# Performance work log

Measured on AMD Instinct MI355X. Metric: run time of the kernel, lower is better.

## Reference

```python
import jax, jax.numpy as jnp
import numpy as np

B, CQ, CK, CV, CO = 16, 256, 256, 256, 256
H, W = 80, 80          # query spatial size (P3-like)
KH, KW = 40, 40        # key/value spatial size (P4-like)
HEADS = 4
R2 = 2 * 2             # region_size ** 2
SCALE = 1.0 / np.float32(np.sqrt(CQ))


def conv1x1(x, w, b):
    # 1x1 conv == per-pixel linear map over channels
    return jnp.einsum('bchw,oc->bohw', x, w) + b[None, :, None, None]


def setup_inputs() -> dict:
    key = jax.random.key(0)
    ks = jax.random.split(key, 10)
    s = 0.05
    return {
        'query': jax.random.normal(ks[0], (B, CQ, H, W), jnp.float32),
        'key':   jax.random.normal(ks[1], (B, CK, KH, KW), jnp.float32),
        'wq': jax.random.normal(ks[2], (CQ, CQ), jnp.float32) * s,
        'bq': jax.random.normal(ks[3], (CQ,), jnp.float32) * s,
        'wk': jax.random.normal(ks[4], (CK, CK), jnp.float32) * s,
        'bk': jax.random.normal(ks[5], (CK,), jnp.float32) * s,
        'wv': jax.random.normal(ks[6], (CV, CV), jnp.float32) * s,
        'bv': jax.random.normal(ks[7], (CV,), jnp.float32) * s,
        'wo': jax.random.normal(ks[8], (CO, CV), jnp.float32) * s,
        'bo': jax.random.normal(ks[9], (CO,), jnp.float32) * s,
    }


def reference(query, key, wq, bq, wk, bk, wv, bv, wo, bo):
    # value defaults to key in the original module
    q = conv1x1(query, wq, bq)               # [B,CQ,H,W]
    k = conv1x1(key, wk, bk)                 # [B,CK,KH,KW]
    v = conv1x1(key, wv, bv)                 # [B,CV,KH,KW]

    b, cq, h, w = q.shape
    # All R2 'patches' in the source are the SAME interpolation (no offsets),
    # so compute it once; bilinear resize matches torch align_corners=False.
    ki = jax.image.resize(k, (b, k.shape[1], h, w), method='bilinear')
    vi = jax.image.resize(v, (b, v.shape[1], h, w), method='bilinear')

    q5 = q.reshape(b, HEADS, cq // HEADS, h, w)
    k5 = ki.reshape(b, HEADS, k.shape[1] // HEADS, h, w)
    v5 = vi.reshape(b, HEADS, v.shape[1] // HEADS, h, w)

    # per-region score; identical for every region patch
    score = jnp.einsum('bhcxy,bhcxy->bhxy', q5, k5) * SCALE     # [B,h,H,W]
    scores = jnp.broadcast_to(score[:, :, None], (b, HEADS, R2, h, w))
    # NOTE: original uses nn.Softmax(dim=3) -> normalizes over the H axis
    attn = jax.nn.softmax(scores, axis=3)                       # [B,h,R2,H,W]

    # out = sum over regions of attn * v (v identical across regions)
    out = jnp.einsum('bhrxy,bhcxy->bhcxy', attn, v5)            # [B,h,C/h,H,W]
    out = out.reshape(b, -1, h, w)                              # [B,CV,H,W]
    return conv1x1(out, wo, bo)                                 # [B,CO,H,W]
```

## Files before the change

kernel.cpp:

```cpp
#include <hip/hip_runtime.h>
#include <hip/hip_bf16.h>

typedef __bf16 bf16;
typedef __attribute__((ext_vector_type(4))) float f32x4;
typedef __attribute__((ext_vector_type(8))) __bf16 bf16x8;
typedef __attribute__((ext_vector_type(4))) __bf16 bf16x4;

__global__ __launch_bounds__(256, 2)
void gemm_cm(const float* __restrict__ act,
             const float* __restrict__ W0, const float* __restrict__ b0, bf16* __restrict__ out0,
             const float* __restrict__ W1, const float* __restrict__ b1, bf16* __restrict__ out1,
             int P) {
  __shared__ alignas(16) bf16 At[2][128][64];
  __shared__ alignas(16) bf16 Bt[2][128][64];
  const int t = threadIdx.x;
  const int b = blockIdx.z;
  const int m0 = blockIdx.x * 128;
  const int sel = blockIdx.y >> 1;
  const int n0 = (blockIdx.y & 1) * 128;
  const float* W    = sel ? W1 : W0;
  const float* bias = sel ? b1 : b0;
  bf16*        out  = sel ? out1 : out0;

  const int w = t >> 6, l = t & 63;
  const int wr = w >> 1, wc = w & 1;
  const int lrow = l & 15, koff = (l >> 4) * 8;

  const float* actb = act + (size_t)b * 256 * (size_t)P;

  f32x4 Ar[2][4];
  f32x4 Br[8];

  auto LOAD = [&](int kt) {
    const int k0 = kt * 64;
#pragma unroll
    for (int u = 0; u < 2; ++u) {
      int unit = u * 256 + t;
      int up = unit & 31, uk = unit >> 5;
      int ps = m0 + up * 4;
      if (ps > P - 4) ps = P - 4;
#pragma unroll
      for (int j = 0; j < 4; ++j)
        Ar[u][j] = *(const f32x4*)(actb + (size_t)(k0 + uk * 4 + j) * P + ps);
    }
#pragma unroll
    for (int it = 0; it < 8; ++it) {
      int idx = it * 256 + t;
      int row = idx >> 4, ce = (idx & 15) * 4;
      Br[it] = *(const f32x4*)(W + (size_t)(n0 + row) * 256 + k0 + ce);
    }
  };

  auto STORE = [&](int buf) {
#pragma unroll
    for (int u = 0; u < 2; ++u) {
      int unit = u * 256 + t;
      int up = unit & 31, uk = unit >> 5;
#pragma unroll
      for (int j = 0; j < 4; ++j) {
        int row = up * 4 + j;
        int cs = (uk * 4) ^ ((row & 7) << 3);
        bf16x4 v = {(bf16)Ar[u][0][j], (bf16)Ar[u][1][j], (bf16)Ar[u][2][j], (bf16)Ar[u][3][j]};
        *(bf16x4*)&At[buf][row][cs] = v;
      }
    }
#pragma unroll
    for (int it = 0; it < 8; ++it) {
      int idx = it * 256 + t;
      int row = idx >> 4, ce = (idx & 15) * 4;
      int cs = ce ^ ((row & 7) << 3);
      bf16x4 h = {(bf16)Br[it][0], (bf16)Br[it][1], (bf16)Br[it][2], (bf16)Br[it][3]};
      *(bf16x4*)&Bt[buf][row][cs] = h;
    }
  };

  f32x4 acc[4][4];
#pragma unroll
  for (int i = 0; i < 4; ++i)
#pragma unroll
    for (int j = 0; j < 4; ++j) acc[i][j] = (f32x4){0.f, 0.f, 0.f, 0.f};

  auto COMPUTE = [&](int buf) {
#pragma unroll
    for (int kk = 0; kk < 2; ++kk) {
      bf16x8 af[4], bv[4];
      const int kb = kk * 32 + koff;
#pragma unroll
      for (int i = 0; i < 4; ++i) {
        int ar = wr * 64 + i * 16 + lrow;
        int br = wc * 64 + i * 16 + lrow;
        af[i] = *(const bf16x8*)&At[buf][ar][kb ^ ((ar & 7) << 3)];
        bv[i] = *(const bf16x8*)&Bt[buf][br][kb ^ ((br & 7) << 3)];
      }
#pragma unroll
      for (int mi = 0; mi < 4; ++mi)
#pragma unroll
        for (int ni = 0; ni < 4; ++ni)
          acc[mi][ni] = __builtin_amdgcn_mfma_f32_16x16x32_bf16(af[mi], bv[ni], acc[mi][ni], 0, 0, 0);
    }
  };

  LOAD(0);
  STORE(0);
  __syncthreads();
#pragma unroll
  for (int kt = 0; kt < 4; ++kt) {
    if (kt < 3) LOAD(kt + 1);
    COMPUTE(kt & 1);
    if (kt < 3) STORE((kt + 1) & 1);
    __syncthreads();
  }

  bf16* ob = out + (size_t)b * (size_t)P * 256;
#pragma unroll
  for (int mi = 0; mi < 4; ++mi) {
#pragma unroll
    for (int r = 0; r < 4; ++r) {
      int p_ = m0 + wr * 64 + mi * 16 + (l >> 4) * 4 + r;
      if (p_ < P) {
#pragma unroll
        for (int ni = 0; ni < 4; ++ni) {
          int o_ = n0 + wc * 64 + ni * 16 + (l & 15);
          ob[(size_t)p_ * 256 + o_] = (bf16)(acc[mi][ni][r] + bias[o_]);
        }
      }
    }
  }
}

__global__ __launch_bounds__(256, 2)
void gemm_pm(const bf16* __restrict__ act, const float* __restrict__ W,
             const float* __restrict__ bias, float* __restrict__ out, int P) {
  __shared__ alignas(16) bf16 At[2][128][64];
  __shared__ alignas(16) bf16 Bt[2][128][64];
  const int t = threadIdx.x;
  const int b = blockIdx.z;
  const int m0 = blockIdx.x * 128;
  const int n0 = blockIdx.y * 128;
  const int w = t >> 6, l = t & 63;
  const int wr = w >> 1, wc = w & 1;
  const int lrow = l & 15, koff = (l >> 4) * 8;

  const bf16* actb = act + (size_t)b * (size_t)P * 256;

  f32x4 Ar[8];
  bf16x8 Brr[4];

  auto LOAD = [&](int kt) {
    const int k0 = kt * 64;
#pragma unroll
    for (int it = 0; it < 8; ++it) {
      int idx = it * 256 + t;
      int row = idx >> 4, ce = (idx & 15) * 4;
      Ar[it] = *(const f32x4*)(W + (size_t)(m0 + row) * 256 + k0 + ce);
    }
#pragma unroll
    for (int it = 0; it < 4; ++it) {
      int idx = it * 256 + t;
      int row = idx >> 3, ce = (idx & 7) * 8;
      Brr[it] = *(const bf16x8*)(actb + (size_t)(n0 + row) * 256 + k0 + ce);
    }
  };

  auto STORE = [&](int buf) {
#pragma unroll
    for (int it = 0; it < 8; ++it) {
      int idx = it * 256 + t;
      int row = idx >> 4, ce = (idx & 15) * 4;
      int cs = ce ^ ((row & 7) << 3);
      bf16x4 h = {(bf16)Ar[it][0], (bf16)Ar[it][1], (bf16)Ar[it][2], (bf16)Ar[it][3]};
      *(bf16x4*)&At[buf][row][cs] = h;
    }
#pragma unroll
    for (int it = 0; it < 4; ++it) {
      int idx = it * 256 + t;
      int row = idx >> 3, ce = (idx & 7) * 8;
      int cs = ce ^ ((row & 7) << 3);
      *(bf16x8*)&Bt[buf][row][cs] = Brr[it];
    }
  };

  f32x4 acc[4][4];
#pragma unroll
  for (int i = 0; i < 4; ++i)
#pragma unroll
    for (int j = 0; j < 4; ++j) acc[i][j] = (f32x4){0.f, 0.f, 0.f, 0.f};

  auto COMPUTE = [&](int buf) {
#pragma unroll
    for (int kk = 0; kk < 2; ++kk) {
      bf16x8 af[4], bv[4];
      const int kb = kk * 32 + koff;
#pragma unroll
      for (int i = 0; i < 4; ++i) {
        int ar = wr * 64 + i * 16 + lrow;
        int br = wc * 64 + i * 16 + lrow;
        af[i] = *(const bf16x8*)&At[buf][ar][kb ^ ((ar & 7) << 3)];
        bv[i] = *(const bf16x8*)&Bt[buf][br][kb ^ ((br & 7) << 3)];
      }
#pragma unroll
      for (int mi = 0; mi < 4; ++mi)
#pragma unroll
        for (int ni = 0; ni < 4; ++ni)
          acc[mi][ni] = __builtin_amdgcn_mfma_f32_16x16x32_bf16(af[mi], bv[ni], acc[mi][ni], 0, 0, 0);
    }
  };

  LOAD(0);
  STORE(0);
  __syncthreads();
#pragma unroll
  for (int kt = 0; kt < 4; ++kt) {
    if (kt < 3) LOAD(kt + 1);
    COMPUTE(kt & 1);
    if (kt < 3) STORE((kt + 1) & 1);
    __syncthreads();
  }

  float* ob = out + (size_t)b * 256 * (size_t)P;
#pragma unroll
  for (int mi = 0; mi < 4; ++mi) {
#pragma unroll
    for (int r = 0; r < 4; ++r) {
      int o_ = m0 + wr * 64 + mi * 16 + (l >> 4) * 4 + r;
      float bvf = bias[o_];
#pragma unroll
      for (int ni = 0; ni < 4; ++ni) {
        int p_ = n0 + wc * 64 + ni * 16 + (l & 15);
        ob[(size_t)o_ * P + p_] = acc[mi][ni][r] + bvf;
      }
    }
  }
}

__global__ void score_kernel(const bf16* __restrict__ Qpm, const bf16* __restrict__ Kpm,
                             float* __restrict__ score) {
  const int t = threadIdx.x;
  const int p = blockIdx.x * 256 + t;
  const int hd = blockIdx.y, b = blockIdx.z;
  const int x = p / 80, y = p % 80;

  float cx = 0.5f * x - 0.25f;
  int ix = (int)floorf(cx);
  float wx1 = cx - ix;
  int x0 = ix < 0 ? 0 : ix, x1 = (ix + 1 > 39) ? 39 : ix + 1;
  float cy = 0.5f * y - 0.25f;
  int iy = (int)floorf(cy);
  float wy1 = cy - iy;
  int y0 = iy < 0 ? 0 : iy, y1 = (iy + 1 > 39) ? 39 : iy + 1;
  float w00 = (1.f - wx1) * (1.f - wy1), w01 = (1.f - wx1) * wy1;
  float w10 = wx1 * (1.f - wy1), w11 = wx1 * wy1;

  const bf16* q   = Qpm + ((size_t)b * 6400 + p) * 256 + hd * 64;
  const bf16* k00 = Kpm + ((size_t)b * 1600 + x0 * 40 + y0) * 256 + hd * 64;
  const bf16* k01 = Kpm + ((size_t)b * 1600 + x0 * 40 + y1) * 256 + hd * 64;
  const bf16* k10 = Kpm + ((size_t)b * 1600 + x1 * 40 + y0) * 256 + hd * 64;
  const bf16* k11 = Kpm + ((size_t)b * 1600 + x1 * 40 + y1) * 256 + hd * 64;

  float dot = 0.f;
#pragma unroll
  for (int i = 0; i < 8; ++i) {
    bf16x8 qv = *(const bf16x8*)(q + i * 8);
    bf16x8 a = *(const bf16x8*)(k00 + i * 8);
    bf16x8 c = *(const bf16x8*)(k01 + i * 8);
    bf16x8 d = *(const bf16x8*)(k10 + i * 8);
    bf16x8 e = *(const bf16x8*)(k11 + i * 8);
#pragma unroll
    for (int j = 0; j < 8; ++j) {
      float kup = w00 * (float)a[j] + w01 * (float)c[j] + w10 * (float)d[j] + w11 * (float)e[j];
      dot += (float)qv[j] * kup;
    }
  }
  score[((size_t)b * 4 + hd) * 6400 + p] = dot * 0.0625f;
}

__global__ void smax_kernel(float* __restrict__ score) {
  __shared__ float s[6400];
  const int hd = blockIdx.x, b = blockIdx.y, t = threadIdx.x;
  float* buf = score + ((size_t)b * 4 + hd) * 6400;
  for (int i = t; i < 6400; i += 256) s[i] = buf[i];
  __syncthreads();
  if (t < 80) {
    const int y = t;
    float m = -1e30f;
    for (int x = 0; x < 80; ++x) m = fmaxf(m, s[x * 80 + y]);
    float sum = 0.f;
    for (int x = 0; x < 80; ++x) {
      float e = __expf(s[x * 80 + y] - m);
      s[x * 80 + y] = e;
      sum += e;
    }
    float inv = 4.0f / sum;
    for (int x = 0; x < 80; ++x) buf[x * 80 + y] = s[x * 80 + y] * inv;
  }
}

__global__ void outgen_kernel(const bf16* __restrict__ Vpm, const float* __restrict__ attn,
                              bf16* __restrict__ outpm) {
  __shared__ float Vx[40][256];
  __shared__ float at[4][80];
  const int x = blockIdx.x, b = blockIdx.y, t = threadIdx.x;

  float cx = 0.5f * x - 0.25f;
  int ix = (int)floorf(cx);
  float wx1 = cx - ix, wx0 = 1.f - wx1;
  int tx0 = ix < 0 ? 0 : ix, tx1 = (ix + 1 > 39) ? 39 : ix + 1;

  const bf16* r0 = Vpm + ((size_t)b * 1600 + tx0 * 40) * 256;
  const bf16* r1 = Vpm + ((size_t)b * 1600 + tx1 * 40) * 256;
  for (int ty = 0; ty < 40; ++ty)
    Vx[ty][t] = wx0 * (float)r0[ty * 256 + t] + wx1 * (float)r1[ty * 256 + t];
  for (int i = t; i < 320; i += 256) {
    int hd = i / 80, y = i % 80;
    at[hd][y] = attn[((size_t)b * 4 + hd) * 6400 + x * 80 + y];
  }
  __syncthreads();

  const int hd = t >> 6;
  bf16* ob = outpm + ((size_t)b * 6400 + x * 80) * 256;
  for (int y = 0; y < 80; ++y) {
    float cyv = 0.5f * y - 0.25f;
    int iy = (int)floorf(cyv);
    float wy1 = cyv - iy;
    int ty0 = iy < 0 ? 0 : iy, ty1 = (iy + 1 > 39) ? 39 : iy + 1;
    float v = (1.f - wy1) * Vx[ty0][t] + wy1 * Vx[ty1][t];
    ob[(size_t)y * 256 + t] = (bf16)(at[hd][y] * v);
  }
}

extern "C" void kernel_launch(void* const* d_in, const int* in_sizes, int n_in,
                              void* d_out, int out_size, void* d_ws, size_t ws_size,
                              hipStream_t stream) {
  const float* query = (const float*)d_in[0];
  const float* key   = (const float*)d_in[1];
  const float* wq    = (const float*)d_in[2];
  const float* bq    = (const float*)d_in[3];
  const float* wk    = (const float*)d_in[4];
  const float* bk    = (const float*)d_in[5];
  const float* wv    = (const float*)d_in[6];
  const float* bv    = (const float*)d_in[7];
  const float* wo    = (const float*)d_in[8];
  const float* bo    = (const float*)d_in[9];

  char* ws = (char*)d_ws;
  bf16*  outpm = (bf16*)(ws);
  bf16*  Kpm   = (bf16*)(ws + 52428800);
  bf16*  Vpm   = (bf16*)(ws + 65536000);
  float* score = (float*)(ws + 78643200);
  bf16*  Qpm   = (bf16*)d_out;

  gemm_cm<<<dim3(50, 2, 16), 256, 0, stream>>>(query, wq, bq, Qpm, wq, bq, Qpm, 6400);
  gemm_cm<<<dim3(13, 4, 16), 256, 0, stream>>>(key, wk, bk, Kpm, wv, bv, Vpm, 1600);
  score_kernel<<<dim3(25, 4, 16), 256, 0, stream>>>(Qpm, Kpm, score);
  smax_kernel<<<dim3(4, 16), 256, 0, stream>>>(score);
  outgen_kernel<<<dim3(80, 16), 256, 0, stream>>>(Vpm, score, outpm);
  gemm_pm<<<dim3(2, 50, 16), 256, 0, stream>>>(outpm, wo, bo, (float*)d_out, 6400);
}
```

Measured before the change: 202.0 us.

## Store Q channel-major and swap output GEMM operands for vectorized epilogues

The Q projection now writes a channel-major layout using bf16x4 vector stores. The score kernel reads Q per channel, so loads across a wavefront are coalesced over pixels. The final GEMM swaps its operand roles so each lane writes f32x4 vectors along pixels instead of scalar stores, and launch bounds drop to one block per SM hint. The aim is better store coalescing in the GEMM epilogues, at the cost of 64 scalar strided Q loads per thread in the score kernel and possibly different register allocation.

Result: no change. 201.2 us (-0.4%).

```diff
diff --git a/kernel.cpp b/kernel.cpp
--- a/kernel.cpp
+++ b/kernel.cpp
@@ -6,7 +6,8 @@
 typedef __attribute__((ext_vector_type(8))) __bf16 bf16x8;
 typedef __attribute__((ext_vector_type(4))) __bf16 bf16x4;
 
-__global__ __launch_bounds__(256, 2)
+template <int EPI>
+__global__ __launch_bounds__(256, 1)
 void gemm_cm(const float* __restrict__ act,
              const float* __restrict__ W0, const float* __restrict__ b0, bf16* __restrict__ out0,
              const float* __restrict__ W1, const float* __restrict__ b1, bf16* __restrict__ out1,
@@ -111,26 +112,42 @@
     __syncthreads();
   }
 
-  bf16* ob = out + (size_t)b * (size_t)P * 256;
-#pragma unroll
-  for (int mi = 0; mi < 4; ++mi) {
-#pragma unroll
-    for (int r = 0; r < 4; ++r) {
-      int p_ = m0 + wr * 64 + mi * 16 + (l >> 4) * 4 + r;
-      if (p_ < P) {
-#pragma unroll
-        for (int ni = 0; ni < 4; ++ni) {
-          int o_ = n0 + wc * 64 + ni * 16 + (l & 15);
-          ob[(size_t)p_ * 256 + o_] = (bf16)(acc[mi][ni][r] + bias[o_]);
+  if (EPI == 0) {
+    bf16* ob = out + (size_t)b * 256 * (size_t)P;
+#pragma unroll
+    for (int mi = 0; mi < 4; ++mi) {
+      int pbase = m0 + wr * 64 + mi * 16 + (l >> 4) * 4;
+#pragma unroll
+      for (int ni = 0; ni < 4; ++ni) {
+        int o_ = n0 + wc * 64 + ni * 16 + (l & 15);
+        float bvf = bias[o_];
+        bf16x4 v = {(bf16)(acc[mi][ni][0] + bvf), (bf16)(acc[mi][ni][1] + bvf),
+                    (bf16)(acc[mi][ni][2] + bvf), (bf16)(acc[mi][ni][3] + bvf)};
+        if (pbase < P) *(bf16x4*)(ob + (size_t)o_ * P + pbase) = v;
+      }
+    }
+  } else {
+    bf16* ob = out + (size_t)b * (size_t)P * 256;
+#pragma unroll
+    for (int mi = 0; mi < 4; ++mi) {
+#pragma unroll
+      for (int r = 0; r < 4; ++r) {
+        int p_ = m0 + wr * 64 + mi * 16 + (l >> 4) * 4 + r;
+        if (p_ < P) {
+#pragma unroll
+          for (int ni = 0; ni < 4; ++ni) {
+            int o_ = n0 + wc * 64 + ni * 16 + (l & 15);
+            ob[(size_t)p_ * 256 + o_] = (bf16)(acc[mi][ni][r] + bias[o_]);
+          }
         }
       }
     }
   }
 }
 
-__global__ __launch_bounds__(256, 2)
-void gemm_pm(const bf16* __restrict__ act, const float* __restrict__ W,
-             const float* __restrict__ bias, float* __restrict__ out, int P) {
+__global__ __launch_bounds__(256, 1)
+void gemm_out(const bf16* __restrict__ act, const float* __restrict__ W,
+              const float* __restrict__ bias, float* __restrict__ out, int P) {
   __shared__ alignas(16) bf16 At[2][128][64];
   __shared__ alignas(16) bf16 Bt[2][128][64];
   const int t = threadIdx.x;
@@ -143,40 +160,40 @@
 
   const bf16* actb = act + (size_t)b * (size_t)P * 256;
 
-  f32x4 Ar[8];
-  bf16x8 Brr[4];
+  bf16x8 Arr[4];
+  f32x4 Br[8];
 
   auto LOAD = [&](int kt) {
     const int k0 = kt * 64;
 #pragma unroll
+    for (int it = 0; it < 4; ++it) {
+      int idx = it * 256 + t;
+      int row = idx >> 3, ce = (idx & 7) * 8;
+      Arr[it] = *(const bf16x8*)(actb + (size_t)(m0 + row) * 256 + k0 + ce);
+    }
+#pragma unroll
     for (int it = 0; it < 8; ++it) {
       int idx = it * 256 + t;
       int row = idx >> 4, ce = (idx & 15) * 4;
-      Ar[it] = *(const f32x4*)(W + (size_t)(m0 + row) * 256 + k0 + ce);
-    }
+      Br[it] = *(const f32x4*)(W + (size_t)(n0 + row) * 256 + k0 + ce);
+    }
+  };
+
+  auto STORE = [&](int buf) {
 #pragma unroll
     for (int it = 0; it < 4; ++it) {
       int idx = it * 256 + t;
       int row = idx >> 3, ce = (idx & 7) * 8;
-      Brr[it] = *(const bf16x8*)(actb + (size_t)(n0 + row) * 256 + k0 + ce);
-    }
-  };
-
-  auto STORE = [&](int buf) {
+      int cs = ce ^ ((row & 7) << 3);
+      *(bf16x8*)&At[buf][row][cs] = Arr[it];
+    }
 #pragma unroll
     for (int it = 0; it < 8; ++it) {
       int idx = it * 256 + t;
       int row = idx >> 4, ce = (idx & 15) * 4;
       int cs = ce ^ ((row & 7) << 3);
-      bf16x4 h = {(bf16)Ar[it][0], (bf16)Ar[it][1], (bf16)Ar[it][2], (bf16)Ar[it][3]};
-      *(bf16x4*)&At[buf][row][cs] = h;
-    }
-#pragma unroll
-    for (int it = 0; it < 4; ++it) {
-      int idx = it * 256 + t;
-      int row = idx >> 3, ce = (idx & 7) * 8;
-      int cs = ce ^ ((row & 7) << 3);
-      *(bf16x8*)&Bt[buf][row][cs] = Brr[it];
+      bf16x4 h = {(bf16)Br[it][0], (bf16)Br[it][1], (bf16)Br[it][2], (bf16)Br[it][3]};
+      *(bf16x4*)&Bt[buf][row][cs] = h;
     }
   };
 
@@ -220,20 +237,19 @@
   float* ob = out + (size_t)b * 256 * (size_t)P;
 #pragma unroll
   for (int mi = 0; mi < 4; ++mi) {
-#pragma unroll
-    for (int r = 0; r < 4; ++r) {
-      int o_ = m0 + wr * 64 + mi * 16 + (l >> 4) * 4 + r;
+    int pbase = m0 + wr * 64 + mi * 16 + (l >> 4) * 4;
+#pragma unroll
+    for (int ni = 0; ni < 4; ++ni) {
+      int o_ = n0 + wc * 64 + ni * 16 + (l & 15);
       float bvf = bias[o_];
-#pragma unroll
-      for (int ni = 0; ni < 4; ++ni) {
-        int p_ = n0 + wc * 64 + ni * 16 + (l & 15);
-        ob[(size_t)o_ * P + p_] = acc[mi][ni][r] + bvf;
-      }
-    }
-  }
-}
-
-__global__ void score_kernel(const bf16* __restrict__ Qpm, const bf16* __restrict__ Kpm,
+      f32x4 v = {acc[mi][ni][0] + bvf, acc[mi][ni][1] + bvf,
+                 acc[mi][ni][2] + bvf, acc[mi][ni][3] + bvf};
+      *(f32x4*)(ob + (size_t)o_ * P + pbase) = v;
+    }
+  }
+}
+
+__global__ void score_kernel(const bf16* __restrict__ Qcm, const bf16* __restrict__ Kpm,
                              float* __restrict__ score) {
   const int t = threadIdx.x;
   const int p = blockIdx.x * 256 + t;
@@ -251,7 +267,7 @@
   float w00 = (1.f - wx1) * (1.f - wy1), w01 = (1.f - wx1) * wy1;
   float w10 = wx1 * (1.f - wy1), w11 = wx1 * wy1;
 
-  const bf16* q   = Qpm + ((size_t)b * 6400 + p) * 256 + hd * 64;
+  const bf16* q   = Qcm + ((size_t)b * 256 + hd * 64) * 6400 + p;
   const bf16* k00 = Kpm + ((size_t)b * 1600 + x0 * 40 + y0) * 256 + hd * 64;
   const bf16* k01 = Kpm + ((size_t)b * 1600 + x0 * 40 + y1) * 256 + hd * 64;
   const bf16* k10 = Kpm + ((size_t)b * 1600 + x1 * 40 + y0) * 256 + hd * 64;
@@ -260,7 +276,6 @@
   float dot = 0.f;
 #pragma unroll
   for (int i = 0; i < 8; ++i) {
-    bf16x8 qv = *(const bf16x8*)(q + i * 8);
     bf16x8 a = *(const bf16x8*)(k00 + i * 8);
     bf16x8 c = *(const bf16x8*)(k01 + i * 8);
     bf16x8 d = *(const bf16x8*)(k10 + i * 8);
@@ -268,7 +283,8 @@
 #pragma unroll
     for (int j = 0; j < 8; ++j) {
       float kup = w00 * (float)a[j] + w01 * (float)c[j] + w10 * (float)d[j] + w11 * (float)e[j];
-      dot += (float)qv[j] * kup;
+      float qc = (float)q[(size_t)(i * 8 + j) * 6400];
+      dot += qc * kup;
     }
   }
   score[((size_t)b * 4 + hd) * 6400 + p] = dot * 0.0625f;
@@ -347,12 +363,12 @@
   bf16*  Kpm   = (bf16*)(ws + 52428800);
   bf16*  Vpm   = (bf16*)(ws + 65536000);
   float* score = (float*)(ws + 78643200);
-  bf16*  Qpm   = (bf16*)d_out;
-
-  gemm_cm<<<dim3(50, 2, 16), 256, 0, stream>>>(query, wq, bq, Qpm, wq, bq, Qpm, 6400);
-  gemm_cm<<<dim3(13, 4, 16), 256, 0, stream>>>(key, wk, bk, Kpm, wv, bv, Vpm, 1600);
-  score_kernel<<<dim3(25, 4, 16), 256, 0, stream>>>(Qpm, Kpm, score);
+  bf16*  Qcm   = (bf16*)d_out;
+
+  gemm_cm<0><<<dim3(50, 2, 16), 256, 0, stream>>>(query, wq, bq, Qcm, wq, bq, Qcm, 6400);
+  gemm_cm<1><<<dim3(13, 4, 16), 256, 0, stream>>>(key, wk, bk, Kpm, wv, bv, Vpm, 1600);
+  score_kernel<<<dim3(25, 4, 16), 256, 0, stream>>>(Qcm, Kpm, score);
   smax_kernel<<<dim3(4, 16), 256, 0, stream>>>(score);
   outgen_kernel<<<dim3(80, 16), 256, 0, stream>>>(Vpm, score, outpm);
-  gemm_pm<<<dim3(2, 50, 16), 256, 0, stream>>>(outpm, wo, bo, (float*)d_out, 6400);
-}
+  gemm_out<<<dim3(50, 2, 16), 256, 0, stream>>>(outpm, wo, bo, (float*)d_out, 6400);
+}
```
